# Kernel tuning notes

Measured on AMD Instinct MI355X. Metric: run time of the kernel, lower is better.

The kernel has to match this reference:

```python
import jax, jax.numpy as jnp
import numpy as np

B, S, D = 2, 2048, 1024
H = 16
DH = D // H  # 64


def setup_inputs() -> dict:
    key = jax.random.key(0)
    ks = jax.random.split(key, 6)
    sc = 0.02
    return {
        "x": jax.random.normal(ks[0], (B, S, D), dtype=jnp.float32),
        "Wq": jax.random.normal(ks[1], (D, D), dtype=jnp.float32) * sc,
        "Wk": jax.random.normal(ks[2], (D, D), dtype=jnp.float32) * sc,
        "Wv": jax.random.normal(ks[3], (D, D), dtype=jnp.float32) * sc,
        "Wo": jax.random.normal(ks[4], (D, D), dtype=jnp.float32) * sc,
        "bo": jnp.zeros((D,), dtype=jnp.float32),
    }


def reference(x, Wq, Wk, Wv, Wo, bo):
    b, s, _ = x.shape
    # project_qkv: Linear (x @ W.T), view to heads, transpose -> [b, H, s, DH]
    def split_heads(t):
        return t.reshape(b, s, H, DH).transpose(0, 2, 1, 3)

    q = split_heads(x @ Wq.T)
    k = split_heads(x @ Wk.T)
    v = split_heads(x @ Wv.T)

    # attn_scores = q @ k^T  [b, H, s, s]
    scores = jnp.einsum("bhqd,bhkd->bhqk", q, k)
    # causal mask: triu(ones, diagonal=1) -> mask out strictly-future positions
    causal = jnp.triu(jnp.ones((s, s), dtype=bool), k=1)
    scores = jnp.where(causal[None, None], -jnp.inf, scores)
    scale = 1.0 / jnp.sqrt(jnp.float32(DH))
    attn = jax.nn.softmax(scores * scale, axis=-1)
    # dropout p=0.0 -> identity
    ctx = jnp.einsum("bhqk,bhkd->bhqd", attn, v)
    # transpose back and flatten heads -> [b, s, D]
    ctx = ctx.transpose(0, 2, 1, 3).reshape(b, s, H * DH)
    return ctx @ Wo.T + bo
```

## Files before the change

### kernel.cpp

```cpp
#include <hip/hip_runtime.h>
#include <stdint.h>

typedef unsigned short u16;
typedef __attribute__((ext_vector_type(8))) short bf16x8;
typedef __attribute__((ext_vector_type(4))) float f32x4;
typedef __attribute__((ext_vector_type(4))) unsigned short u16x4;

__device__ __forceinline__ u16 f2bf(float f) {
  union { float f; uint32_t u; } c; c.f = f;
  uint32_t u = c.u;
  return (u16)((u + 0x7fffu + ((u >> 16) & 1u)) >> 16);
}

__device__ __forceinline__ uint32_t pk_bf16(float lo, float hi) {
  uint32_t d;
  asm("v_cvt_pk_bf16_f32 %0, %1, %2" : "=v"(d) : "v"(lo), "v"(hi));
  return d;
}

__device__ __forceinline__ void gload_lds16(const u16* g, u16* l) {
  __builtin_amdgcn_global_load_lds(
      (const __attribute__((address_space(1))) void*)g,
      (__attribute__((address_space(3))) void*)l, 16, 0, 0);
}

__global__ void cast_f32_bf16(const float* __restrict__ src, u16* __restrict__ dst, int n) {
  int i = (blockIdx.x * blockDim.x + threadIdx.x) * 4;
  int stride = gridDim.x * blockDim.x * 4;
  for (; i < n; i += stride) {
    float4 v = *reinterpret_cast<const float4*>(src + i);
    u16x4 o = { f2bf(v.x), f2bf(v.y), f2bf(v.z), f2bf(v.w) };
    *reinterpret_cast<u16x4*>(dst + i) = o;
  }
}

__global__ void cast_weights(const float* __restrict__ Wq, const float* __restrict__ Wk,
                             const float* __restrict__ Wv, const float* __restrict__ Wo,
                             u16* __restrict__ Wcat, u16* __restrict__ Wob) {
  int i = (blockIdx.x * blockDim.x + threadIdx.x) * 4;
  int stride = gridDim.x * blockDim.x * 4;
  for (; i < 4194304; i += stride) {
    const int sel = i >> 20;
    const int off = i & 1048575;
    const float* src = (sel == 0) ? Wq : (sel == 1) ? Wk : (sel == 2) ? Wv : Wo;
    float4 v = *reinterpret_cast<const float4*>(src + off);
    u16x4 o = { f2bf(v.x), f2bf(v.y), f2bf(v.z), f2bf(v.w) };
    u16* dst = (sel < 3) ? (Wcat + i) : (Wob + off);
    *reinterpret_cast<u16x4*>(dst) = o;
  }
}

#define QSCALE 0.18033688011112042f

template<int EPI>
__global__ __launch_bounds__(256) void gemm_bt(
    const u16* __restrict__ A, const u16* __restrict__ B,
    int M, int N, int K,
    u16* __restrict__ o0, u16* __restrict__ o1, u16* __restrict__ o2,
    float* __restrict__ fo, const float* __restrict__ bias)
{
  __shared__ __align__(16) u16 As[2][128 * 32];
  __shared__ __align__(16) u16 Bs[2][128 * 32];
  const int tid = threadIdx.x;
  const int w = tid >> 6, l = tid & 63;
  const int m0 = blockIdx.y * 128, n0 = blockIdx.x * 128;
  const int arow = (w << 4) + (l >> 2);
  const int acol = (l & 3) << 3;
  const int wr = (w >> 1) << 6, wc = (w & 1) << 6;
  const int lr = l & 15, hi = l >> 4;
  const int lk = hi << 3;
  f32x4 acc[4][4] = {};

  const u16* Ap = A + (size_t)(m0 + arow) * K + acol;
  const u16* Bp = B + (size_t)(n0 + arow) * K + acol;
  const int so = (w << 9);

  gload_lds16(Ap, &As[0][so]);
  gload_lds16(Ap + (size_t)64 * K, &As[0][so + 2048]);
  gload_lds16(Bp, &Bs[0][so]);
  gload_lds16(Bp + (size_t)64 * K, &Bs[0][so + 2048]);

  int buf = 0;
  for (int k0 = 0; k0 < K; k0 += 32) {
    if (k0 + 32 < K) {
      const int nb = buf ^ 1;
      gload_lds16(Ap + k0 + 32, &As[nb][so]);
      gload_lds16(Ap + (size_t)64 * K + k0 + 32, &As[nb][so + 2048]);
      gload_lds16(Bp + k0 + 32, &Bs[nb][so]);
      gload_lds16(Bp + (size_t)64 * K + k0 + 32, &Bs[nb][so + 2048]);
      asm volatile("s_waitcnt vmcnt(4)" ::: "memory");
    } else {
      asm volatile("s_waitcnt vmcnt(0)" ::: "memory");
    }
    __builtin_amdgcn_sched_barrier(0);
    __builtin_amdgcn_s_barrier();
    bf16x8 af[4], bfr[4];
#pragma unroll
    for (int m = 0; m < 4; ++m)
      af[m] = *(const bf16x8*)(&As[buf][0] + (wr + m * 16 + lr) * 32 + lk);
#pragma unroll
    for (int n = 0; n < 4; ++n)
      bfr[n] = *(const bf16x8*)(&Bs[buf][0] + (wc + n * 16 + lr) * 32 + lk);
    __builtin_amdgcn_s_setprio(1);
#pragma unroll
    for (int m = 0; m < 4; ++m)
#pragma unroll
      for (int n = 0; n < 4; ++n)
        acc[m][n] = __builtin_amdgcn_mfma_f32_16x16x32_bf16(af[m], bfr[n], acc[m][n], 0, 0, 0);
    __builtin_amdgcn_s_setprio(0);
    __builtin_amdgcn_s_barrier();
    buf ^= 1;
  }

#pragma unroll
  for (int mm = 0; mm < 4; ++mm) {
#pragma unroll
    for (int nn = 0; nn < 4; ++nn) {
      const int ng = n0 + wc + nn * 16 + lr;
      if (EPI == 0) {
        const int mat = ng >> 10;
        const int col = ng & 1023;
        const int h = col >> 6, dh = col & 63;
#pragma unroll
        for (int r = 0; r < 4; ++r) {
          const int mg = m0 + wr + mm * 16 + (hi << 2) + r;
          const int b = mg >> 11, s = mg & 2047;
          if (mat == 0)
            o0[(((size_t)(b * 16 + h)) * 2048 + s) * 64 + dh] = f2bf(acc[mm][nn][r] * QSCALE);
          else if (mat == 1)
            o1[(((size_t)(b * 16 + h)) * 2048 + s) * 64 + dh] = f2bf(acc[mm][nn][r]);
          else
            o2[(((size_t)(b * 16 + h)) * 64 + dh) * 2048 + s] = f2bf(acc[mm][nn][r]);
        }
      } else {
        const float bv = bias[ng];
#pragma unroll
        for (int r = 0; r < 4; ++r) {
          const int mg = m0 + wr + mm * 16 + (hi << 2) + r;
          fo[(size_t)mg * N + ng] = acc[mm][nn][r] + bv;
        }
      }
    }
  }
}

__global__ __launch_bounds__(256) void flash_attn(
    const u16* __restrict__ Qg, const u16* __restrict__ Kg,
    const u16* __restrict__ Vtg, u16* __restrict__ ctx)
{
  __shared__ __align__(16) u16 Ks[2][4096];
  __shared__ __align__(16) u16 Vts[2][4096];
  __shared__ __align__(16) u16 PT[4][1024];
  const int tid = threadIdx.x, w = tid >> 6, l = tid & 63;
  const int lr = l & 15, hi = l >> 4;
  const int x = blockIdx.x, y = blockIdx.y;
  const int xi = (x + y) & 31;
  const int qt = (xi & 1) ? (31 - (xi >> 1)) : (xi >> 1);
  const int bh = y;
  const size_t kqbase = (size_t)bh * (2048 * 64);
  const int q0 = qt * 64;
  const int nkt = qt + 1;

  bf16x8 qf[2];
  {
    const u16* qp = Qg + kqbase + (size_t)(q0 + w * 16 + lr) * 64 + hi * 8;
    qf[0] = *(const bf16x8*)(qp);
    qf[1] = *(const bf16x8*)(qp + 32);
  }

  const int c0 = (w * 2 + 0) * 64 + l;
  const int c1 = (w * 2 + 1) * 64 + l;
  const int r0 = c0 >> 3, p0 = c0 & 7;
  const int r1 = c1 >> 3, p1 = c1 & 7;
  const u16* kg0 = Kg + kqbase + r0 * 64 + ((p0 ^ (r0 & 7)) << 3);
  const u16* kg1 = Kg + kqbase + r1 * 64 + ((p1 ^ (r1 & 7)) << 3);
  const u16* vg0 = Vtg + kqbase + r0 * 2048 + ((p0 ^ (r0 & 7)) << 3);
  const u16* vg1 = Vtg + kqbase + r1 * 2048 + ((p1 ^ (r1 & 7)) << 3);
  u16* kd0 = (u16*)&Ks[0][(w * 2 + 0) * 512];
  u16* kd1 = (u16*)&Ks[0][(w * 2 + 1) * 512];
  u16* vd0 = (u16*)&Vts[0][(w * 2 + 0) * 512];
  u16* vd1 = (u16*)&Vts[0][(w * 2 + 1) * 512];

  f32x4 acc[4] = {};
  float lsum = 0.0f;
  const int qg = q0 + w * 16 + lr;

  gload_lds16(kg0, kd0);
  gload_lds16(kg1, kd1);
  gload_lds16(vg0, vd0);
  gload_lds16(vg1, vd1);

  int buf = 0;
  for (int kt = 0; kt < nkt; ++kt) {
    if (kt + 1 < nkt) {
      const int nb = (buf ^ 1) * 4096;
      gload_lds16(kg0 + (size_t)(kt + 1) * 4096, kd0 + nb);
      gload_lds16(kg1 + (size_t)(kt + 1) * 4096, kd1 + nb);
      gload_lds16(vg0 + (kt + 1) * 64, vd0 + nb);
      gload_lds16(vg1 + (kt + 1) * 64, vd1 + nb);
      asm volatile("s_waitcnt vmcnt(8)" ::: "memory");
    } else {
      asm volatile("s_waitcnt vmcnt(0)" ::: "memory");
    }
    __builtin_amdgcn_sched_barrier(0);
    __builtin_amdgcn_s_barrier();
    {
      const u16* ksb = &Ks[buf][0];
      const u16* vsb = &Vts[buf][0];
      f32x4 sv[4];
      __builtin_amdgcn_s_setprio(1);
#pragma unroll
      for (int cf = 0; cf < 4; ++cf) {
        f32x4 z = {};
#pragma unroll
        for (int ch = 0; ch < 2; ++ch) {
          const int krow = cf * 16 + lr;
          const int boff = ((krow << 7) + ((ch * 32 + hi * 8) << 1)) ^ ((krow & 7) << 4);
          bf16x8 kf = *(const bf16x8*)((const char*)ksb + boff);
          z = __builtin_amdgcn_mfma_f32_16x16x32_bf16(kf, qf[ch], z, 0, 0, 0);
        }
        sv[cf] = z;
      }
      __builtin_amdgcn_s_setprio(0);

      const bool diag = (kt == nkt - 1);
      const int kb = kt * 64 + hi * 4;
      float ts = 0.0f;
#pragma unroll
      for (int cf = 0; cf < 4; ++cf) {
        f32x4 pv;
#pragma unroll
        for (int r = 0; r < 4; ++r) {
          float s = sv[cf][r];
          if (diag && (kb + cf * 16 + r) > qg) s = -1e30f;
          pv[r] = exp2f(s);
        }
        sv[cf] = pv;
        ts += (pv[0] + pv[1]) + (pv[2] + pv[3]);
      }
      lsum += ts;

      {
        const int rowb = lr << 7;
        const int swz = (lr & 7) << 4;
#pragma unroll
        for (int cf = 0; cf < 4; ++cf) {
          uint32_t d0 = pk_bf16(sv[cf][0], sv[cf][1]);
          uint32_t d1 = pk_bf16(sv[cf][2], sv[cf][3]);
          uint2 val = { d0, d1 };
          const int boff = (rowb + ((cf * 16 + hi * 4) << 1)) ^ swz;
          *(uint2*)((char*)&PT[w][0] + boff) = val;
        }
      }

#pragma unroll
      for (int ch = 0; ch < 2; ++ch) {
        const int boffp = ((lr << 7) + (ch * 64 + hi * 16)) ^ ((lr & 7) << 4);
        bf16x8 pa = *(const bf16x8*)((const char*)&PT[w][0] + boffp);
        __builtin_amdgcn_s_setprio(1);
#pragma unroll
        for (int df = 0; df < 4; ++df) {
          const int vrow = df * 16 + lr;
          const int boffv = ((vrow << 7) + ((ch * 32 + hi * 8) << 1)) ^ ((vrow & 7) << 4);
          bf16x8 vf = *(const bf16x8*)((const char*)vsb + boffv);
          acc[df] = __builtin_amdgcn_mfma_f32_16x16x32_bf16(pa, vf, acc[df], 0, 0, 0);
        }
        __builtin_amdgcn_s_setprio(0);
      }
    }
    __builtin_amdgcn_s_barrier();
    buf ^= 1;
  }

  float lf = lsum;
  lf += __shfl_xor(lf, 16);
  lf += __shfl_xor(lf, 32);
  const int h = bh & 15, b = bh >> 4;
#pragma unroll
  for (int r = 0; r < 4; ++r) {
    const float inv = 1.0f / __shfl(lf, hi * 4 + r);
    const int s = q0 + w * 16 + hi * 4 + r;
    const size_t rowbase = ((size_t)(b * 2048 + s)) * 1024 + h * 64;
#pragma unroll
    for (int df = 0; df < 4; ++df)
      ctx[rowbase + df * 16 + lr] = f2bf(acc[df][r] * inv);
  }
}

extern "C" void kernel_launch(void* const* d_in, const int* in_sizes, int n_in,
                              void* d_out, int out_size, void* d_ws, size_t ws_size,
                              hipStream_t stream) {
  const float* x  = (const float*)d_in[0];
  const float* Wq = (const float*)d_in[1];
  const float* Wk = (const float*)d_in[2];
  const float* Wv = (const float*)d_in[3];
  const float* Wo = (const float*)d_in[4];
  const float* bo = (const float*)d_in[5];
  float* out = (float*)d_out;

  const size_t MB = 1ull << 20;
  if (ws_size < 48 * MB) return;
  char* ws = (char*)d_ws;
  u16* xb   = (u16*)(ws);
  u16* Wcat = (u16*)(ws + 8 * MB);
  u16* Wob  = (u16*)(ws + 14 * MB);
  u16* Qb   = (u16*)(ws + 16 * MB);
  u16* Kb   = (u16*)(ws + 24 * MB);
  u16* Vtb  = (u16*)(ws + 32 * MB);
  u16* ctxb = (u16*)(ws + 40 * MB);

  hipLaunchKernelGGL(cast_f32_bf16, dim3(2048), dim3(256), 0, stream, x, xb, 4194304);
  hipLaunchKernelGGL(cast_weights, dim3(2048), dim3(256), 0, stream,
                     Wq, Wk, Wv, Wo, Wcat, Wob);

  hipLaunchKernelGGL((gemm_bt<0>), dim3(24, 32), dim3(256), 0, stream,
                     xb, Wcat, 4096, 3072, 1024, Qb, Kb, Vtb, (float*)nullptr, (const float*)nullptr);
  hipLaunchKernelGGL(flash_attn, dim3(32, 32), dim3(256), 0, stream, Qb, Kb, Vtb, ctxb);
  hipLaunchKernelGGL((gemm_bt<1>), dim3(8, 32), dim3(256), 0, stream,
                     ctxb, Wob, 4096, 1024, 1024,
                     (u16*)nullptr, (u16*)nullptr, (u16*)nullptr, out, bo);
}
```

Baseline: 142.0 us.

## Load K/V directly to registers in flash attention with 32-row per-wave Q tiles

Flash attention stops staging K and V through double-buffered shared memory and has each wave load its K/V fragments straight from global memory into registers. This removes the workgroup barriers. Each wave now handles 32 query rows (two 16-row fragments) instead of 16, so every K/V fragment feeds twice as many MFMAs. Each wave also computes its own causal tile count. The grid becomes a 1D launch of 512 blocks covering 128 query rows each, with a new head/q-tile mapping for load balance. In exchange, global/L2 traffic per wave rises because the 4 waves of a block no longer share staged K/V, and register pressure grows.

```diff
diff --git a/kernel.cpp b/kernel.cpp
--- a/kernel.cpp
+++ b/kernel.cpp
@@ -148,142 +148,132 @@
     const u16* __restrict__ Qg, const u16* __restrict__ Kg,
     const u16* __restrict__ Vtg, u16* __restrict__ ctx)
 {
-  __shared__ __align__(16) u16 Ks[2][4096];
-  __shared__ __align__(16) u16 Vts[2][4096];
-  __shared__ __align__(16) u16 PT[4][1024];
+  __shared__ __align__(16) u16 PT[4][2048];
   const int tid = threadIdx.x, w = tid >> 6, l = tid & 63;
   const int lr = l & 15, hi = l >> 4;
-  const int x = blockIdx.x, y = blockIdx.y;
-  const int xi = (x + y) & 31;
-  const int qt = (xi & 1) ? (31 - (xi >> 1)) : (xi >> 1);
-  const int bh = y;
+  const int wg = blockIdx.x;
+  const int bhi = (wg >> 3) & 3;
+  const int qslot = wg >> 5;
+  const int bh = (wg & 7) + (bhi << 3);
+  const int qt = (bhi & 1) ? (15 - qslot) : qslot;
   const size_t kqbase = (size_t)bh * (2048 * 64);
-  const int q0 = qt * 64;
-  const int nkt = qt + 1;
-
-  bf16x8 qf[2];
+  const int q0 = qt * 128 + w * 32;
+  const int nkt = (q0 >> 6) + 1;
+
+  bf16x8 qf[2][2];
   {
-    const u16* qp = Qg + kqbase + (size_t)(q0 + w * 16 + lr) * 64 + hi * 8;
-    qf[0] = *(const bf16x8*)(qp);
-    qf[1] = *(const bf16x8*)(qp + 32);
-  }
-
-  const int c0 = (w * 2 + 0) * 64 + l;
-  const int c1 = (w * 2 + 1) * 64 + l;
-  const int r0 = c0 >> 3, p0 = c0 & 7;
-  const int r1 = c1 >> 3, p1 = c1 & 7;
-  const u16* kg0 = Kg + kqbase + r0 * 64 + ((p0 ^ (r0 & 7)) << 3);
-  const u16* kg1 = Kg + kqbase + r1 * 64 + ((p1 ^ (r1 & 7)) << 3);
-  const u16* vg0 = Vtg + kqbase + r0 * 2048 + ((p0 ^ (r0 & 7)) << 3);
-  const u16* vg1 = Vtg + kqbase + r1 * 2048 + ((p1 ^ (r1 & 7)) << 3);
-  u16* kd0 = (u16*)&Ks[0][(w * 2 + 0) * 512];
-  u16* kd1 = (u16*)&Ks[0][(w * 2 + 1) * 512];
-  u16* vd0 = (u16*)&Vts[0][(w * 2 + 0) * 512];
-  u16* vd1 = (u16*)&Vts[0][(w * 2 + 1) * 512];
-
-  f32x4 acc[4] = {};
-  float lsum = 0.0f;
-  const int qg = q0 + w * 16 + lr;
-
-  gload_lds16(kg0, kd0);
-  gload_lds16(kg1, kd1);
-  gload_lds16(vg0, vd0);
-  gload_lds16(vg1, vd1);
-
-  int buf = 0;
+    const u16* qp = Qg + kqbase + (size_t)(q0 + lr) * 64 + hi * 8;
+#pragma unroll
+    for (int qr = 0; qr < 2; ++qr) {
+      qf[qr][0] = *(const bf16x8*)(qp + qr * 1024);
+      qf[qr][1] = *(const bf16x8*)(qp + qr * 1024 + 32);
+    }
+  }
+
+  const u16* kp = Kg + kqbase + lr * 64 + hi * 8;
+  const u16* vp = Vtg + kqbase + (size_t)lr * 2048 + hi * 8;
+
+  f32x4 acc[2][4] = {};
+  float lsum[2] = {0.0f, 0.0f};
+  const int swz = (lr & 7) << 4;
+
   for (int kt = 0; kt < nkt; ++kt) {
-    if (kt + 1 < nkt) {
-      const int nb = (buf ^ 1) * 4096;
-      gload_lds16(kg0 + (size_t)(kt + 1) * 4096, kd0 + nb);
-      gload_lds16(kg1 + (size_t)(kt + 1) * 4096, kd1 + nb);
-      gload_lds16(vg0 + (kt + 1) * 64, vd0 + nb);
-      gload_lds16(vg1 + (kt + 1) * 64, vd1 + nb);
-      asm volatile("s_waitcnt vmcnt(8)" ::: "memory");
-    } else {
-      asm volatile("s_waitcnt vmcnt(0)" ::: "memory");
-    }
-    __builtin_amdgcn_sched_barrier(0);
-    __builtin_amdgcn_s_barrier();
-    {
-      const u16* ksb = &Ks[buf][0];
-      const u16* vsb = &Vts[buf][0];
-      f32x4 sv[4];
-      __builtin_amdgcn_s_setprio(1);
-#pragma unroll
-      for (int cf = 0; cf < 4; ++cf) {
-        f32x4 z = {};
-#pragma unroll
-        for (int ch = 0; ch < 2; ++ch) {
-          const int krow = cf * 16 + lr;
-          const int boff = ((krow << 7) + ((ch * 32 + hi * 8) << 1)) ^ ((krow & 7) << 4);
-          bf16x8 kf = *(const bf16x8*)((const char*)ksb + boff);
-          z = __builtin_amdgcn_mfma_f32_16x16x32_bf16(kf, qf[ch], z, 0, 0, 0);
-        }
-        sv[cf] = z;
-      }
-      __builtin_amdgcn_s_setprio(0);
-
-      const bool diag = (kt == nkt - 1);
-      const int kb = kt * 64 + hi * 4;
+    const u16* kpt = kp + (size_t)kt * 4096;
+    bf16x8 kf[4][2];
+#pragma unroll
+    for (int cf = 0; cf < 4; ++cf) {
+      kf[cf][0] = *(const bf16x8*)(kpt + cf * 1024);
+      kf[cf][1] = *(const bf16x8*)(kpt + cf * 1024 + 32);
+    }
+    f32x4 sv[2][4];
+    __builtin_amdgcn_s_setprio(1);
+#pragma unroll
+    for (int cf = 0; cf < 4; ++cf) {
+      f32x4 z0 = {}, z1 = {};
+#pragma unroll
+      for (int ch = 0; ch < 2; ++ch) {
+        z0 = __builtin_amdgcn_mfma_f32_16x16x32_bf16(kf[cf][ch], qf[0][ch], z0, 0, 0, 0);
+        z1 = __builtin_amdgcn_mfma_f32_16x16x32_bf16(kf[cf][ch], qf[1][ch], z1, 0, 0, 0);
+      }
+      sv[0][cf] = z0; sv[1][cf] = z1;
+    }
+    __builtin_amdgcn_s_setprio(0);
+
+    const u16* vpt = vp + kt * 64;
+    bf16x8 vf[4][2];
+#pragma unroll
+    for (int df = 0; df < 4; ++df) {
+      vf[df][0] = *(const bf16x8*)(vpt + df * 32768);
+      vf[df][1] = *(const bf16x8*)(vpt + df * 32768 + 32);
+    }
+
+    const bool diag = (kt == nkt - 1);
+    const int kb = kt * 64 + hi * 4;
+#pragma unroll
+    for (int qr = 0; qr < 2; ++qr) {
+      const int qg = q0 + qr * 16 + lr;
       float ts = 0.0f;
 #pragma unroll
       for (int cf = 0; cf < 4; ++cf) {
         f32x4 pv;
 #pragma unroll
         for (int r = 0; r < 4; ++r) {
-          float s = sv[cf][r];
+          float s = sv[qr][cf][r];
           if (diag && (kb + cf * 16 + r) > qg) s = -1e30f;
           pv[r] = exp2f(s);
         }
-        sv[cf] = pv;
+        sv[qr][cf] = pv;
         ts += (pv[0] + pv[1]) + (pv[2] + pv[3]);
       }
-      lsum += ts;
-
-      {
-        const int rowb = lr << 7;
-        const int swz = (lr & 7) << 4;
-#pragma unroll
-        for (int cf = 0; cf < 4; ++cf) {
-          uint32_t d0 = pk_bf16(sv[cf][0], sv[cf][1]);
-          uint32_t d1 = pk_bf16(sv[cf][2], sv[cf][3]);
-          uint2 val = { d0, d1 };
-          const int boff = (rowb + ((cf * 16 + hi * 4) << 1)) ^ swz;
-          *(uint2*)((char*)&PT[w][0] + boff) = val;
-        }
-      }
-
-#pragma unroll
-      for (int ch = 0; ch < 2; ++ch) {
-        const int boffp = ((lr << 7) + (ch * 64 + hi * 16)) ^ ((lr & 7) << 4);
-        bf16x8 pa = *(const bf16x8*)((const char*)&PT[w][0] + boffp);
-        __builtin_amdgcn_s_setprio(1);
-#pragma unroll
-        for (int df = 0; df < 4; ++df) {
-          const int vrow = df * 16 + lr;
-          const int boffv = ((vrow << 7) + ((ch * 32 + hi * 8) << 1)) ^ ((vrow & 7) << 4);
-          bf16x8 vf = *(const bf16x8*)((const char*)vsb + boffv);
-          acc[df] = __builtin_amdgcn_mfma_f32_16x16x32_bf16(pa, vf, acc[df], 0, 0, 0);
-        }
-        __builtin_amdgcn_s_setprio(0);
-      }
-    }
-    __builtin_amdgcn_s_barrier();
-    buf ^= 1;
-  }
-
-  float lf = lsum;
-  lf += __shfl_xor(lf, 16);
-  lf += __shfl_xor(lf, 32);
+      lsum[qr] += ts;
+    }
+
+#pragma unroll
+    for (int qr = 0; qr < 2; ++qr) {
+      const int rowb = (qr * 16 + lr) << 7;
+#pragma unroll
+      for (int cf = 0; cf < 4; ++cf) {
+        uint32_t d0 = pk_bf16(sv[qr][cf][0], sv[qr][cf][1]);
+        uint32_t d1 = pk_bf16(sv[qr][cf][2], sv[qr][cf][3]);
+        uint2 val = { d0, d1 };
+        const int boff = (rowb + ((cf * 16 + hi * 4) << 1)) ^ swz;
+        *(uint2*)((char*)&PT[w][0] + boff) = val;
+      }
+    }
+
+#pragma unroll
+    for (int ch = 0; ch < 2; ++ch) {
+      bf16x8 pa[2];
+#pragma unroll
+      for (int qr = 0; qr < 2; ++qr) {
+        const int boffp = (((qr * 16 + lr) << 7) + (ch * 64 + hi * 16)) ^ swz;
+        pa[qr] = *(const bf16x8*)((const char*)&PT[w][0] + boffp);
+      }
+      __builtin_amdgcn_s_setprio(1);
+#pragma unroll
+      for (int df = 0; df < 4; ++df) {
+        acc[0][df] = __builtin_amdgcn_mfma_f32_16x16x32_bf16(pa[0], vf[df][ch], acc[0][df], 0, 0, 0);
+        acc[1][df] = __builtin_amdgcn_mfma_f32_16x16x32_bf16(pa[1], vf[df][ch], acc[1][df], 0, 0, 0);
+      }
+      __builtin_amdgcn_s_setprio(0);
+    }
+  }
+
   const int h = bh & 15, b = bh >> 4;
 #pragma unroll
-  for (int r = 0; r < 4; ++r) {
-    const float inv = 1.0f / __shfl(lf, hi * 4 + r);
-    const int s = q0 + w * 16 + hi * 4 + r;
-    const size_t rowbase = ((size_t)(b * 2048 + s)) * 1024 + h * 64;
-#pragma unroll
-    for (int df = 0; df < 4; ++df)
-      ctx[rowbase + df * 16 + lr] = f2bf(acc[df][r] * inv);
+  for (int qr = 0; qr < 2; ++qr) {
+    float t = lsum[qr];
+    t += __shfl_xor(t, 16);
+    t += __shfl_xor(t, 32);
+#pragma unroll
+    for (int r = 0; r < 4; ++r) {
+      const float inv = 1.0f / __shfl(t, hi * 4 + r);
+      const int s = q0 + qr * 16 + hi * 4 + r;
+      const size_t rowbase = ((size_t)(b * 2048 + s)) * 1024 + h * 64;
+#pragma unroll
+      for (int df = 0; df < 4; ++df)
+        ctx[rowbase + df * 16 + lr] = f2bf(acc[qr][df][r] * inv);
+    }
   }
 }
 
@@ -315,7 +305,7 @@
 
   hipLaunchKernelGGL((gemm_bt<0>), dim3(24, 32), dim3(256), 0, stream,
                      xb, Wcat, 4096, 3072, 1024, Qb, Kb, Vtb, (float*)nullptr, (const float*)nullptr);
-  hipLaunchKernelGGL(flash_attn, dim3(32, 32), dim3(256), 0, stream, Qb, Kb, Vtb, ctxb);
+  hipLaunchKernelGGL(flash_attn, dim3(512), dim3(256), 0, stream, Qb, Kb, Vtb, ctxb);
   hipLaunchKernelGGL((gemm_bt<1>), dim3(8, 32), dim3(256), 0, stream,
                      ctxb, Wob, 4096, 1024, 1024,
                      (u16*)nullptr, (u16*)nullptr, (u16*)nullptr, out, bo);
```

Measured after the change: 168.7 us. 1.19x slower.

## Process two 64-key subtiles per pipeline stage in causal flash attention

Applied to the files above, without the earlier changes.

Each stage of the double-buffered loop now loads and consumes 128 keys as two 64-key subtiles, which halves the number of loop iterations and block-wide barriers. Subtiles past the diagonal are skipped with an early break, and the causal mask now uses the subtile index. The cost is double the LDS staging (about 72KB per block instead of 40KB), which can cut resident blocks per CU and reduce latency hiding. Some K/V data for a subtile that is never used may also be fetched.

```diff
diff --git a/kernel.cpp b/kernel.cpp
--- a/kernel.cpp
+++ b/kernel.cpp
@@ -148,8 +148,8 @@
     const u16* __restrict__ Qg, const u16* __restrict__ Kg,
     const u16* __restrict__ Vtg, u16* __restrict__ ctx)
 {
-  __shared__ __align__(16) u16 Ks[2][4096];
-  __shared__ __align__(16) u16 Vts[2][4096];
+  __shared__ __align__(16) u16 Ks[2][2][4096];
+  __shared__ __align__(16) u16 Vts[2][2][4096];
   __shared__ __align__(16) u16 PT[4][1024];
   const int tid = threadIdx.x, w = tid >> 6, l = tid & 63;
   const int lr = l & 15, hi = l >> 4;
@@ -159,7 +159,7 @@
   const int bh = y;
   const size_t kqbase = (size_t)bh * (2048 * 64);
   const int q0 = qt * 64;
-  const int nkt = qt + 1;
+  const int nkt = (qt + 2) >> 1;
 
   bf16x8 qf[2];
   {
@@ -174,39 +174,51 @@
   const int r1 = c1 >> 3, p1 = c1 & 7;
   const u16* kg0 = Kg + kqbase + r0 * 64 + ((p0 ^ (r0 & 7)) << 3);
   const u16* kg1 = Kg + kqbase + r1 * 64 + ((p1 ^ (r1 & 7)) << 3);
-  const u16* vg0 = Vtg + kqbase + r0 * 2048 + ((p0 ^ (r0 & 7)) << 3);
-  const u16* vg1 = Vtg + kqbase + r1 * 2048 + ((p1 ^ (r1 & 7)) << 3);
-  u16* kd0 = (u16*)&Ks[0][(w * 2 + 0) * 512];
-  u16* kd1 = (u16*)&Ks[0][(w * 2 + 1) * 512];
-  u16* vd0 = (u16*)&Vts[0][(w * 2 + 0) * 512];
-  u16* vd1 = (u16*)&Vts[0][(w * 2 + 1) * 512];
+  const u16* vg0 = Vtg + kqbase + (size_t)r0 * 2048 + ((p0 ^ (r0 & 7)) << 3);
+  const u16* vg1 = Vtg + kqbase + (size_t)r1 * 2048 + ((p1 ^ (r1 & 7)) << 3);
+  u16* kd0 = &Ks[0][0][(w * 2 + 0) * 512];
+  u16* kd1 = &Ks[0][0][(w * 2 + 1) * 512];
+  u16* vd0 = &Vts[0][0][(w * 2 + 0) * 512];
+  u16* vd1 = &Vts[0][0][(w * 2 + 1) * 512];
 
   f32x4 acc[4] = {};
   float lsum = 0.0f;
   const int qg = q0 + w * 16 + lr;
 
-  gload_lds16(kg0, kd0);
-  gload_lds16(kg1, kd1);
-  gload_lds16(vg0, vd0);
-  gload_lds16(vg1, vd1);
+#pragma unroll
+  for (int s = 0; s < 2; ++s) {
+    gload_lds16(kg0 + s * 4096, kd0 + s * 4096);
+    gload_lds16(kg1 + s * 4096, kd1 + s * 4096);
+    gload_lds16(vg0 + s * 64,  vd0 + s * 4096);
+    gload_lds16(vg1 + s * 64,  vd1 + s * 4096);
+  }
 
   int buf = 0;
   for (int kt = 0; kt < nkt; ++kt) {
     if (kt + 1 < nkt) {
-      const int nb = (buf ^ 1) * 4096;
-      gload_lds16(kg0 + (size_t)(kt + 1) * 4096, kd0 + nb);
-      gload_lds16(kg1 + (size_t)(kt + 1) * 4096, kd1 + nb);
-      gload_lds16(vg0 + (kt + 1) * 64, vd0 + nb);
-      gload_lds16(vg1 + (kt + 1) * 64, vd1 + nb);
+      const int nb = (buf ^ 1) * 8192;
+      const size_t ko = (size_t)(kt + 1) * 8192;
+      const int vo = (kt + 1) * 128;
+#pragma unroll
+      for (int s = 0; s < 2; ++s) {
+        gload_lds16(kg0 + ko + s * 4096, kd0 + nb + s * 4096);
+        gload_lds16(kg1 + ko + s * 4096, kd1 + nb + s * 4096);
+        gload_lds16(vg0 + vo + s * 64,  vd0 + nb + s * 4096);
+        gload_lds16(vg1 + vo + s * 64,  vd1 + nb + s * 4096);
+      }
       asm volatile("s_waitcnt vmcnt(8)" ::: "memory");
     } else {
       asm volatile("s_waitcnt vmcnt(0)" ::: "memory");
     }
     __builtin_amdgcn_sched_barrier(0);
     __builtin_amdgcn_s_barrier();
-    {
-      const u16* ksb = &Ks[buf][0];
-      const u16* vsb = &Vts[buf][0];
+
+#pragma unroll
+    for (int s = 0; s < 2; ++s) {
+      const int sub = 2 * kt + s;
+      if (sub > qt) break;
+      const u16* ksb = &Ks[buf][s][0];
+      const u16* vsb = &Vts[buf][s][0];
       f32x4 sv[4];
       __builtin_amdgcn_s_setprio(1);
 #pragma unroll
@@ -223,17 +235,17 @@
       }
       __builtin_amdgcn_s_setprio(0);
 
-      const bool diag = (kt == nkt - 1);
-      const int kb = kt * 64 + hi * 4;
+      const bool diag = (sub == qt);
+      const int kb = sub * 64 + hi * 4;
       float ts = 0.0f;
 #pragma unroll
       for (int cf = 0; cf < 4; ++cf) {
         f32x4 pv;
 #pragma unroll
         for (int r = 0; r < 4; ++r) {
-          float s = sv[cf][r];
-          if (diag && (kb + cf * 16 + r) > qg) s = -1e30f;
-          pv[r] = exp2f(s);
+          float sc = sv[cf][r];
+          if (diag && (kb + cf * 16 + r) > qg) sc = -1e30f;
+          pv[r] = exp2f(sc);
         }
         sv[cf] = pv;
         ts += (pv[0] + pv[1]) + (pv[2] + pv[3]);
```

After: 162.3 us. 1.14x slower.

## Use 256x256 four-stage QKV GEMM, merge cast kernels, tighten attention waitcnt

Applied to the files above, without the earlier changes.

Replaces the 128x128 QKV projection GEMM with a 512-thread 256x256-tile kernel. It uses a four-buffer, two-ahead global-to-LDS prefetch pipeline and XOR-swizzled LDS layouts, aiming for more reuse per loaded tile and better latency hiding. The separate x and weight cast kernels are merged into one launch to cut launch overhead. In flash attention, the vmcnt wait is changed from 8 to 4 so the current tile's loads are actually complete before use, and the V offsets are widened to size_t. The large tile uses about 128KB of LDS and launches only 192 blocks, which may underfill the GPU's CUs.

```diff
diff --git a/kernel.cpp b/kernel.cpp
--- a/kernel.cpp
+++ b/kernel.cpp
@@ -24,39 +24,133 @@
       (__attribute__((address_space(3))) void*)l, 16, 0, 0);
 }
 
-__global__ void cast_f32_bf16(const float* __restrict__ src, u16* __restrict__ dst, int n) {
+__global__ void cast_all(const float* __restrict__ x,
+                         const float* __restrict__ Wq, const float* __restrict__ Wk,
+                         const float* __restrict__ Wv, const float* __restrict__ Wo,
+                         u16* __restrict__ xb, u16* __restrict__ Wcat, u16* __restrict__ Wob) {
   int i = (blockIdx.x * blockDim.x + threadIdx.x) * 4;
-  int stride = gridDim.x * blockDim.x * 4;
-  for (; i < n; i += stride) {
-    float4 v = *reinterpret_cast<const float4*>(src + i);
+  const int stride = gridDim.x * blockDim.x * 4;
+  for (; i < 8388608; i += stride) {
+    const float* src;
+    u16* dst;
+    if (i < 4194304) {
+      src = x + i; dst = xb + i;
+    } else {
+      const int j = i - 4194304;
+      const int sel = j >> 20, off = j & 1048575;
+      src = ((sel == 0) ? Wq : (sel == 1) ? Wk : (sel == 2) ? Wv : Wo) + off;
+      dst = (sel < 3) ? (Wcat + j) : (Wob + off);
+    }
+    float4 v = *reinterpret_cast<const float4*>(src);
     u16x4 o = { f2bf(v.x), f2bf(v.y), f2bf(v.z), f2bf(v.w) };
-    *reinterpret_cast<u16x4*>(dst + i) = o;
-  }
-}
-
-__global__ void cast_weights(const float* __restrict__ Wq, const float* __restrict__ Wk,
-                             const float* __restrict__ Wv, const float* __restrict__ Wo,
-                             u16* __restrict__ Wcat, u16* __restrict__ Wob) {
-  int i = (blockIdx.x * blockDim.x + threadIdx.x) * 4;
-  int stride = gridDim.x * blockDim.x * 4;
-  for (; i < 4194304; i += stride) {
-    const int sel = i >> 20;
-    const int off = i & 1048575;
-    const float* src = (sel == 0) ? Wq : (sel == 1) ? Wk : (sel == 2) ? Wv : Wo;
-    float4 v = *reinterpret_cast<const float4*>(src + off);
-    u16x4 o = { f2bf(v.x), f2bf(v.y), f2bf(v.z), f2bf(v.w) };
-    u16* dst = (sel < 3) ? (Wcat + i) : (Wob + off);
     *reinterpret_cast<u16x4*>(dst) = o;
   }
 }
 
 #define QSCALE 0.18033688011112042f
 
-template<int EPI>
-__global__ __launch_bounds__(256) void gemm_bt(
+__global__ __launch_bounds__(512, 2) void gemm256(
+    const u16* __restrict__ A, const u16* __restrict__ B,
+    u16* __restrict__ o0, u16* __restrict__ o1, u16* __restrict__ o2)
+{
+  const int K = 1024;
+  __shared__ __align__(16) u16 As[4][256 * 32];
+  __shared__ __align__(16) u16 Bs[4][256 * 32];
+  const int tid = threadIdx.x;
+  const int w = tid >> 6, l = tid & 63;
+  const int wm = w >> 2, wn = w & 3;
+  const int lr = l & 15, hi = l >> 4;
+  const int m0 = blockIdx.y * 256, n0 = blockIdx.x * 256;
+
+  const int c0 = tid, c1 = tid + 512;
+  const int r0 = c0 >> 2, s0 = c0 & 3;
+  const int r1 = c1 >> 2, s1 = c1 & 3;
+  const u16* Ag0 = A + (size_t)(m0 + r0) * K + (s0 ^ ((r0 >> 1) & 3)) * 8;
+  const u16* Ag1 = A + (size_t)(m0 + r1) * K + (s1 ^ ((r1 >> 1) & 3)) * 8;
+  const u16* Bg0 = B + (size_t)(n0 + r0) * K + (s0 ^ ((r0 >> 1) & 3)) * 8;
+  const u16* Bg1 = B + (size_t)(n0 + r1) * K + (s1 ^ ((r1 >> 1) & 3)) * 8;
+
+  f32x4 acc[8][4] = {};
+
+  int aoff[8], boff[4];
+#pragma unroll
+  for (int mf = 0; mf < 8; ++mf) {
+    const int row = wm * 128 + mf * 16 + lr;
+    aoff[mf] = row * 64 + ((hi ^ ((row >> 1) & 3)) << 4);
+  }
+#pragma unroll
+  for (int nf = 0; nf < 4; ++nf) {
+    const int row = wn * 64 + nf * 16 + lr;
+    boff[nf] = row * 64 + ((hi ^ ((row >> 1) & 3)) << 4);
+  }
+
+#pragma unroll
+  for (int s = 0; s < 2; ++s) {
+    gload_lds16(Ag0 + s * 32, &As[s][c0 * 8]);
+    gload_lds16(Ag1 + s * 32, &As[s][c1 * 8]);
+    gload_lds16(Bg0 + s * 32, &Bs[s][c0 * 8]);
+    gload_lds16(Bg1 + s * 32, &Bs[s][c1 * 8]);
+  }
+
+  for (int s = 0; s < 32; ++s) {
+    if (s + 2 < 32) {
+      const int rg = (s + 2) & 3;
+      gload_lds16(Ag0 + (s + 2) * 32, &As[rg][c0 * 8]);
+      gload_lds16(Ag1 + (s + 2) * 32, &As[rg][c1 * 8]);
+      gload_lds16(Bg0 + (s + 2) * 32, &Bs[rg][c0 * 8]);
+      gload_lds16(Bg1 + (s + 2) * 32, &Bs[rg][c1 * 8]);
+      asm volatile("s_waitcnt vmcnt(8)" ::: "memory");
+    } else if (s + 1 < 32) {
+      asm volatile("s_waitcnt vmcnt(4)" ::: "memory");
+    } else {
+      asm volatile("s_waitcnt vmcnt(0)" ::: "memory");
+    }
+    __builtin_amdgcn_sched_barrier(0);
+    __builtin_amdgcn_s_barrier();
+    const char* as = (const char*)&As[s & 3][0];
+    const char* bs = (const char*)&Bs[s & 3][0];
+    bf16x8 af[8], bfr[4];
+#pragma unroll
+    for (int mf = 0; mf < 8; ++mf)
+      af[mf] = *(const bf16x8*)(as + aoff[mf]);
+#pragma unroll
+    for (int nf = 0; nf < 4; ++nf)
+      bfr[nf] = *(const bf16x8*)(bs + boff[nf]);
+    __builtin_amdgcn_s_setprio(1);
+#pragma unroll
+    for (int mf = 0; mf < 8; ++mf)
+#pragma unroll
+      for (int nf = 0; nf < 4; ++nf)
+        acc[mf][nf] = __builtin_amdgcn_mfma_f32_16x16x32_bf16(af[mf], bfr[nf], acc[mf][nf], 0, 0, 0);
+    __builtin_amdgcn_s_setprio(0);
+    __builtin_amdgcn_s_barrier();
+  }
+
+#pragma unroll
+  for (int mf = 0; mf < 8; ++mf)
+#pragma unroll
+    for (int nf = 0; nf < 4; ++nf) {
+      const int ng = n0 + wn * 64 + nf * 16 + lr;
+      const int mat = ng >> 10;
+      const int col = ng & 1023;
+      const int h = col >> 6, dh = col & 63;
+#pragma unroll
+      for (int r = 0; r < 4; ++r) {
+        const int mg = m0 + wm * 128 + mf * 16 + hi * 4 + r;
+        const int b = mg >> 11, sq = mg & 2047;
+        if (mat == 0)
+          o0[(((size_t)(b * 16 + h)) * 2048 + sq) * 64 + dh] = f2bf(acc[mf][nf][r] * QSCALE);
+        else if (mat == 1)
+          o1[(((size_t)(b * 16 + h)) * 2048 + sq) * 64 + dh] = f2bf(acc[mf][nf][r]);
+        else
+          o2[(((size_t)(b * 16 + h)) * 64 + dh) * 2048 + sq] = f2bf(acc[mf][nf][r]);
+      }
+    }
+}
+
+__global__ __launch_bounds__(256) void gemm_out(
     const u16* __restrict__ A, const u16* __restrict__ B,
     int M, int N, int K,
-    u16* __restrict__ o0, u16* __restrict__ o1, u16* __restrict__ o2,
     float* __restrict__ fo, const float* __restrict__ bias)
 {
   __shared__ __align__(16) u16 As[2][128 * 32];
@@ -113,35 +207,17 @@
   }
 
 #pragma unroll
-  for (int mm = 0; mm < 4; ++mm) {
+  for (int mm = 0; mm < 4; ++mm)
 #pragma unroll
     for (int nn = 0; nn < 4; ++nn) {
       const int ng = n0 + wc + nn * 16 + lr;
-      if (EPI == 0) {
-        const int mat = ng >> 10;
-        const int col = ng & 1023;
-        const int h = col >> 6, dh = col & 63;
-#pragma unroll
-        for (int r = 0; r < 4; ++r) {
-          const int mg = m0 + wr + mm * 16 + (hi << 2) + r;
-          const int b = mg >> 11, s = mg & 2047;
-          if (mat == 0)
-            o0[(((size_t)(b * 16 + h)) * 2048 + s) * 64 + dh] = f2bf(acc[mm][nn][r] * QSCALE);
-          else if (mat == 1)
-            o1[(((size_t)(b * 16 + h)) * 2048 + s) * 64 + dh] = f2bf(acc[mm][nn][r]);
-          else
-            o2[(((size_t)(b * 16 + h)) * 64 + dh) * 2048 + s] = f2bf(acc[mm][nn][r]);
-        }
-      } else {
-        const float bv = bias[ng];
-#pragma unroll
-        for (int r = 0; r < 4; ++r) {
-          const int mg = m0 + wr + mm * 16 + (hi << 2) + r;
-          fo[(size_t)mg * N + ng] = acc[mm][nn][r] + bv;
-        }
-      }
-    }
-  }
+      const float bv = bias[ng];
+#pragma unroll
+      for (int r = 0; r < 4; ++r) {
+        const int mg = m0 + wr + mm * 16 + (hi << 2) + r;
+        fo[(size_t)mg * N + ng] = acc[mm][nn][r] + bv;
+      }
+    }
 }
 
 __global__ __launch_bounds__(256) void flash_attn(
@@ -174,8 +250,8 @@
   const int r1 = c1 >> 3, p1 = c1 & 7;
   const u16* kg0 = Kg + kqbase + r0 * 64 + ((p0 ^ (r0 & 7)) << 3);
   const u16* kg1 = Kg + kqbase + r1 * 64 + ((p1 ^ (r1 & 7)) << 3);
-  const u16* vg0 = Vtg + kqbase + r0 * 2048 + ((p0 ^ (r0 & 7)) << 3);
-  const u16* vg1 = Vtg + kqbase + r1 * 2048 + ((p1 ^ (r1 & 7)) << 3);
+  const u16* vg0 = Vtg + kqbase + (size_t)r0 * 2048 + ((p0 ^ (r0 & 7)) << 3);
+  const u16* vg1 = Vtg + kqbase + (size_t)r1 * 2048 + ((p1 ^ (r1 & 7)) << 3);
   u16* kd0 = (u16*)&Ks[0][(w * 2 + 0) * 512];
   u16* kd1 = (u16*)&Ks[0][(w * 2 + 1) * 512];
   u16* vd0 = (u16*)&Vts[0][(w * 2 + 0) * 512];
@@ -198,7 +274,7 @@
       gload_lds16(kg1 + (size_t)(kt + 1) * 4096, kd1 + nb);
       gload_lds16(vg0 + (kt + 1) * 64, vd0 + nb);
       gload_lds16(vg1 + (kt + 1) * 64, vd1 + nb);
-      asm volatile("s_waitcnt vmcnt(8)" ::: "memory");
+      asm volatile("s_waitcnt vmcnt(4)" ::: "memory");
     } else {
       asm volatile("s_waitcnt vmcnt(0)" ::: "memory");
     }
@@ -309,14 +385,11 @@
   u16* Vtb  = (u16*)(ws + 32 * MB);
   u16* ctxb = (u16*)(ws + 40 * MB);
 
-  hipLaunchKernelGGL(cast_f32_bf16, dim3(2048), dim3(256), 0, stream, x, xb, 4194304);
-  hipLaunchKernelGGL(cast_weights, dim3(2048), dim3(256), 0, stream,
-                     Wq, Wk, Wv, Wo, Wcat, Wob);
-
-  hipLaunchKernelGGL((gemm_bt<0>), dim3(24, 32), dim3(256), 0, stream,
-                     xb, Wcat, 4096, 3072, 1024, Qb, Kb, Vtb, (float*)nullptr, (const float*)nullptr);
+  hipLaunchKernelGGL(cast_all, dim3(4096), dim3(256), 0, stream,
+                     x, Wq, Wk, Wv, Wo, xb, Wcat, Wob);
+  hipLaunchKernelGGL(gemm256, dim3(12, 16), dim3(512), 0, stream,
+                     xb, Wcat, Qb, Kb, Vtb);
   hipLaunchKernelGGL(flash_attn, dim3(32, 32), dim3(256), 0, stream, Qb, Kb, Vtb, ctxb);
-  hipLaunchKernelGGL((gemm_bt<1>), dim3(8, 32), dim3(256), 0, stream,
-                     ctxb, Wob, 4096, 1024, 1024,
-                     (u16*)nullptr, (u16*)nullptr, (u16*)nullptr, out, bo);
-}
+  hipLaunchKernelGGL(gemm_out, dim3(8, 32), dim3(256), 0, stream,
+                     ctxb, Wob, 4096, 1024, 1024, out, bo);
+}
```

Result: slower. 163.8 us (+15.4%).
